# Optimization experiments

Hardware: AMD Instinct MI355X
Metric: run time of the kernel (lower is better)

The kernel has to match this reference:

```python
import jax, jax.numpy as jnp
import numpy as np

DIM = 1536; NH = 12; HD = 128; C2 = HD // 2          # rope half-dim = 64
F, H, W = 1, 30, 52
FRAME = H * W                                         # 1560 tokens/frame
SINK_FRAMES = 1; LOCAL_ATTN = 6
SINK = SINK_FRAMES * FRAME                            # 1560
MAX_ATTN = LOCAL_ATTN * 1560                          # 9360
CACHE = 9360                                          # kv cache length
GLOBAL_END = 9360; LOCAL_END_CACHE = 9360             # cache state before step
SPLITS = (C2 - 2 * (C2 // 3), C2 // 3, C2 // 3)       # (22, 21, 21)
EPS = 1e-6


def setup_inputs() -> dict:
    key = jax.random.key(0)
    ks = jax.random.split(key, 12)
    s = F * H * W
    rn = lambda k, sh, sc=1.0: jax.random.normal(k, sh, jnp.float32) * sc
    x = rn(ks[0], (1, s, DIM))
    Wq = rn(ks[1], (DIM, DIM), 0.02); Wk = rn(ks[2], (DIM, DIM), 0.02)
    Wv = rn(ks[3], (DIM, DIM), 0.02); Wo = rn(ks[4], (DIM, DIM), 0.02)
    zb = jnp.zeros((DIM,), jnp.float32)
    angles = jax.random.uniform(ks[5], (1024, C2), jnp.float32) * (2.0 * np.pi)
    freqs_cos = jnp.cos(angles); freqs_sin = jnp.sin(angles)
    cache_k = rn(ks[6], (1, CACHE, NH, HD)); cache_v = rn(ks[7], (1, CACHE, NH, HD))
    return dict(x=x, Wq=Wq, bq=zb, Wk=Wk, bk=zb, Wv=Wv, bv=zb, Wo=Wo, bo=zb,
                nq_w=jnp.ones((DIM,), jnp.float32), nk_w=jnp.ones((DIM,), jnp.float32),
                cache_k=cache_k, cache_v=cache_v,
                freqs_cos=freqs_cos, freqs_sin=freqs_sin,
                seq_lens=jnp.array([s], jnp.int32),
                grid_sizes=jnp.array([[F, H, W]], jnp.int32),
                current_start=GLOBAL_END)


def _rmsnorm(x, w):
    return x * jax.lax.rsqrt(jnp.mean(x * x, -1, keepdims=True) + EPS) * w


def _grid_table(table, start_frame):
    """table [1024, C2] -> per-token rope factors [S, 1, C2] over the (F,H,W) grid."""
    s0, s1, s2 = SPLITS
    tf, th, tw = table[:, :s0], table[:, s0:s0 + s1], table[:, s0 + s1:]
    fp = jnp.broadcast_to(tf[start_frame:start_frame + F][:, None, None, :], (F, H, W, s0))
    hp = jnp.broadcast_to(th[:H][None, :, None, :], (F, H, W, s1))
    wp = jnp.broadcast_to(tw[:W][None, None, :, :], (F, H, W, s2))
    return jnp.concatenate([fp, hp, wp], -1).reshape(F * H * W, 1, C2)


def _rope(x, cos, sin):
    # x: [b, s, n, d]; cos/sin: [s, 1, C2] (complex multiply in real arithmetic)
    b, s, n, d = x.shape
    xp = x.reshape(b, s, n, d // 2, 2)
    xr, xi = xp[..., 0], xp[..., 1]
    c, sn = cos[None], sin[None]                      # [1, s, 1, C2]
    out_r = xr * c - xi * sn
    out_i = xr * sn + xi * c
    return jnp.stack([out_r, out_i], -1).reshape(b, s, n, d)


def reference(x, Wq, bq, Wk, bk, Wv, bv, Wo, bo, nq_w, nk_w,
              cache_k, cache_v, freqs_cos, freqs_sin,
              seq_lens, grid_sizes, current_start):
    b, s = x.shape[:2]
    q = _rmsnorm(x @ Wq.T + bq, nq_w).reshape(b, s, NH, HD)
    k = _rmsnorm(x @ Wk.T + bk, nk_w).reshape(b, s, NH, HD)
    v = (x @ Wv.T + bv).reshape(b, s, NH, HD)

    start_frame = int(current_start) // FRAME
    cos = _grid_table(freqs_cos, start_frame)
    sin = _grid_table(freqs_sin, start_frame)
    rq = _rope(q, cos, sin)
    rk = _rope(k, cos, sin)

    # --- static cache bookkeeping (roll_and_insert path; all Python ints) ---
    num_new = s
    current_end = int(current_start) + num_new
    num_evicted = num_new + LOCAL_END_CACHE - CACHE           # 1560
    num_rolled = LOCAL_END_CACHE - num_evicted - SINK         # 6240
    local_end = LOCAL_END_CACHE + current_end - GLOBAL_END - num_evicted  # 9360
    local_start = local_end - num_new                         # 7800 == SINK + num_rolled
    temp_k = jnp.concatenate(
        [cache_k[:, :SINK], cache_k[:, SINK + num_evicted:SINK + num_evicted + num_rolled], rk], axis=1)
    temp_v = jnp.concatenate(
        [cache_v[:, :SINK], cache_v[:, SINK + num_evicted:SINK + num_evicted + num_rolled], v], axis=1)

    # --- sink + sliding-window attention ---
    local_budget = MAX_ATTN - SINK
    win_start = max(SINK, local_end - local_budget)
    k_cat = jnp.concatenate([temp_k[:, :SINK], temp_k[:, win_start:local_end]], axis=1)
    v_cat = jnp.concatenate([temp_v[:, :SINK], temp_v[:, win_start:local_end]], axis=1)

    logits = jnp.einsum('bqhd,bkhd->bhqk', rq, k_cat) * (HD ** -0.5)
    probs = jax.nn.softmax(logits, axis=-1)
    out = jnp.einsum('bhqk,bkhd->bqhd', probs, v_cat)
    y = out.reshape(b, s, DIM) @ Wo.T + bo
    return y
```

## Files before the change

### kernel.cpp

```cpp
#include <hip/hip_runtime.h>
#include <hip/hip_bf16.h>

typedef __bf16 bf16;
typedef __bf16 bf16x2 __attribute__((ext_vector_type(2)));
typedef __bf16 bf16x4 __attribute__((ext_vector_type(4)));
typedef __bf16 bf16x8 __attribute__((ext_vector_type(8)));
typedef float f32x4 __attribute__((ext_vector_type(4)));
typedef float f32x16 __attribute__((ext_vector_type(16)));
typedef unsigned u32x2 __attribute__((ext_vector_type(2)));

#define DIM 1536
#define NH 12
#define HD 128
#define SEQ 1560
#define KV 9360
#define KVP 9408
#define SINK 1560
#define NEWBASE 7800
#define QSCALE_L2E (0.08838834764831845f * 1.4426950408889634f)
#define NSPLIT 6
#define CHUNK 1568
#define NT 49
#define KB 32
#define QBLK 128
#define NQT 13

__device__ __forceinline__ void gl_lds16(const void* g, void* l) {
  __builtin_amdgcn_global_load_lds(
      (const __attribute__((address_space(1))) unsigned int*)g,
      (__attribute__((address_space(3))) unsigned int*)l, 16, 0, 0);
}

__device__ __forceinline__ f32x16 mfma32(bf16x8 a, bf16x8 b, f32x16 c) {
  return __builtin_amdgcn_mfma_f32_32x32x16_bf16(a, b, c, 0, 0, 0);
}

struct CastBatch {
  const float* src[5];
  bf16* dst[5];
  int n[5];
};
__global__ __launch_bounds__(256) void castall(CastBatch cb) {
  const float* src = cb.src[blockIdx.y];
  bf16* dst = cb.dst[blockIdx.y];
  int n = cb.n[blockIdx.y];
  int i = (blockIdx.x * 256 + threadIdx.x) * 8;
  if (i < n) {
    float4 a = *(const float4*)(src + i);
    float4 b = *(const float4*)(src + i + 4);
    bf16x8 o;
    o[0] = (bf16)a.x; o[1] = (bf16)a.y; o[2] = (bf16)a.z; o[3] = (bf16)a.w;
    o[4] = (bf16)b.x; o[5] = (bf16)b.y; o[6] = (bf16)b.z; o[7] = (bf16)b.w;
    *(bf16x8*)(dst + i) = o;
  }
}

__global__ __launch_bounds__(256) void clear_pad(bf16* __restrict__ Kcat,
                                                 bf16* __restrict__ Vt) {
  int h = blockIdx.y;
  int i = blockIdx.x * 256 + threadIdx.x;
  if (i < (KVP - KV) * HD) {
    int r = KV + i / HD, d = i % HD;
    Kcat[((size_t)h * KVP + r) * HD + d] = (bf16)0.f;
    int dv = i / (KVP - KV), j = KV + i % (KVP - KV);
    Vt[((size_t)h * HD + dv) * KVP + j] = (bf16)0.f;
  }
}

struct GemmBatch {
  const bf16* B[3];
  const float* bias[3];
  float* C[3];
};

#define BM 128
#define BN 128
#define BK 32

__global__ __launch_bounds__(256, 2) void gemm_bt(const bf16* __restrict__ A,
                                                  GemmBatch gb, int M) {
  const bf16* Bw = gb.B[blockIdx.z];
  const float* bias = gb.bias[blockIdx.z];
  float* C = gb.C[blockIdx.z];
  int bm = blockIdx.x * BM;
  int bn = blockIdx.y * BN;

  __shared__ bf16 Alds[2][BM][BK];
  __shared__ bf16 Blds[2][BN][BK];

  int t = threadIdx.x;
  int lane = t & 63;
  int wave = t >> 6;
  int wr = wave >> 1, wc = wave & 1;
  int fr = lane & 15;
  int fo = (lane >> 4) * 8;

  f32x4 acc[4][4] = {};

  const int NK = DIM / BK;
  int colA = (lane & 3) * 8;
  int lrow = lane >> 2;

#define STAGEG(buf, k0)                                                     \
  {                                                                         \
    _Pragma("unroll") for (int p = 0; p < 2; ++p) {                         \
      int rbase = wave * 16 + p * 64;                                       \
      int ga = bm + rbase + lrow;                                           \
      if (ga > M - 1) ga = M - 1;                                           \
      gl_lds16(A + (size_t)ga * DIM + (k0) + colA, &Alds[buf][rbase][0]);   \
      int gbv = bn + rbase + lrow;                                          \
      gl_lds16(Bw + (size_t)gbv * DIM + (k0) + colA, &Blds[buf][rbase][0]); \
    }                                                                       \
  }

  STAGEG(0, 0);
  int cur = 0;
  for (int ks = 0; ks < NK; ++ks) {
    __syncthreads();
    if (ks + 1 < NK) STAGEG(cur ^ 1, (ks + 1) * BK);
    bf16x8 af[4], bfv[4];
#pragma unroll
    for (int i = 0; i < 4; ++i)
      af[i] = *(const bf16x8*)&Alds[cur][wr * 64 + i * 16 + fr][fo];
#pragma unroll
    for (int j = 0; j < 4; ++j)
      bfv[j] = *(const bf16x8*)&Blds[cur][wc * 64 + j * 16 + fr][fo];
#pragma unroll
    for (int i = 0; i < 4; ++i)
#pragma unroll
      for (int j = 0; j < 4; ++j)
        acc[i][j] = __builtin_amdgcn_mfma_f32_16x16x32_bf16(af[i], bfv[j],
                                                            acc[i][j], 0, 0, 0);
    cur ^= 1;
  }
#undef STAGEG

  int g4 = (lane >> 4) * 4;
#pragma unroll
  for (int i = 0; i < 4; ++i) {
    int mbase = bm + wr * 64 + i * 16 + g4;
#pragma unroll
    for (int j = 0; j < 4; ++j) {
      int col = bn + wc * 64 + j * 16 + fr;
      float bv = bias[col];
#pragma unroll
      for (int r = 0; r < 4; ++r) {
        int m = mbase + r;
        if (m < M) C[(size_t)m * DIM + col] = acc[i][j][r] + bv;
      }
    }
  }
}

__global__ __launch_bounds__(256) void norm_rope(
    const float* __restrict__ qraw, const float* __restrict__ kraw,
    const float* __restrict__ nqw, const float* __restrict__ nkw,
    const float* __restrict__ fcos, const float* __restrict__ fsin,
    bf16* __restrict__ Qh, bf16* __restrict__ Kcat) {
  int tok = blockIdx.x;
  int tid = threadIdx.x;
  const float* qr = qraw + (size_t)tok * DIM;
  const float* kr = kraw + (size_t)tok * DIM;
  float sq = 0.f, sk = 0.f;
  for (int c = tid; c < DIM; c += 256) {
    float a = qr[c];
    sq += a * a;
    float b = kr[c];
    sk += b * b;
  }
#pragma unroll
  for (int off = 32; off; off >>= 1) {
    sq += __shfl_down(sq, off);
    sk += __shfl_down(sk, off);
  }
  __shared__ float red[2][4];
  int w = tid >> 6;
  if ((tid & 63) == 0) {
    red[0][w] = sq;
    red[1][w] = sk;
  }
  __syncthreads();
  sq = red[0][0] + red[0][1] + red[0][2] + red[0][3];
  sk = red[1][0] + red[1][1] + red[1][2] + red[1][3];
  float rsq = rsqrtf(sq * (1.0f / DIM) + 1e-6f);
  float rsk = rsqrtf(sk * (1.0f / DIM) + 1e-6f);

  int hrow = tok / 52, wrow = tok % 52;
  for (int p = tid; p < NH * 64; p += 256) {
    int n = p >> 6, i = p & 63;
    int trow = (i < 22) ? 6 : (i < 43 ? hrow : wrow);
    float cs = fcos[trow * 64 + i];
    float sn = fsin[trow * 64 + i];
    int c = n * HD + 2 * i;
    float xr = qr[c] * rsq * nqw[c];
    float xi = qr[c + 1] * rsq * nqw[c + 1];
    bf16x2 qo;
    qo[0] = (bf16)((xr * cs - xi * sn) * QSCALE_L2E);
    qo[1] = (bf16)((xr * sn + xi * cs) * QSCALE_L2E);
    *(bf16x2*)(Qh + ((size_t)n * SEQ + tok) * HD + 2 * i) = qo;
    float yr = kr[c] * rsk * nkw[c];
    float yi = kr[c + 1] * rsk * nkw[c + 1];
    bf16x2 ko;
    ko[0] = (bf16)(yr * cs - yi * sn);
    ko[1] = (bf16)(yr * sn + yi * cs);
    *(bf16x2*)(Kcat + ((size_t)n * KVP + NEWBASE + tok) * HD + 2 * i) = ko;
  }
}

__global__ __launch_bounds__(256) void build_kcat(const float* __restrict__ cache_k,
                                                  bf16* __restrict__ Kcat) {
  int j = blockIdx.x;
  int src = j < SINK ? j : j + SINK;
  const float* sp = cache_k + (size_t)src * DIM;
  for (int c4 = threadIdx.x; c4 < DIM / 4; c4 += 256) {
    float4 v = *(const float4*)(sp + c4 * 4);
    int c = c4 * 4;
    int n = c >> 7, d = c & 127;
    bf16x4 o;
    o[0] = (bf16)v.x; o[1] = (bf16)v.y; o[2] = (bf16)v.z; o[3] = (bf16)v.w;
    *(bf16x4*)(Kcat + ((size_t)n * KVP + j) * HD + d) = o;
  }
}

__global__ __launch_bounds__(256) void build_vt(const float* __restrict__ cache_v,
                                                const float* __restrict__ vraw,
                                                bf16* __restrict__ Vt) {
  int h = blockIdx.y;
  int j0 = blockIdx.x * 64;
  __shared__ bf16 T[128][72];
  int tid = threadIdx.x;
  for (int idx = tid; idx < 64 * 32; idx += 256) {
    int jl = idx >> 5, s = idx & 31;
    int j = j0 + jl;
    if (j >= KV) continue;
    const float* sp;
    if (j < NEWBASE) {
      int srcj = j < SINK ? j : j + SINK;
      sp = cache_v + (size_t)srcj * DIM + h * HD;
    } else {
      sp = vraw + (size_t)(j - NEWBASE) * DIM + h * HD;
    }
    float4 v = *(const float4*)(sp + s * 4);
    T[s * 4 + 0][jl] = (bf16)v.x;
    T[s * 4 + 1][jl] = (bf16)v.y;
    T[s * 4 + 2][jl] = (bf16)v.z;
    T[s * 4 + 3][jl] = (bf16)v.w;
  }
  __syncthreads();
  for (int idx = tid; idx < 128 * 16; idx += 256) {
    int d = idx >> 4, g = idx & 15;
    int j = j0 + g * 4;
    if (j + 4 > KV) continue;
    bf16x4 o;
    o[0] = T[d][4 * g];
    o[1] = T[d][4 * g + 1];
    o[2] = T[d][4 * g + 2];
    o[3] = T[d][4 * g + 3];
    *(bf16x4*)(Vt + ((size_t)h * HD + d) * KVP + j) = o;
  }
}

__global__ __launch_bounds__(256, 3) void attn_split(const bf16* __restrict__ Qh,
                                                     const bf16* __restrict__ Kcat,
                                                     const bf16* __restrict__ Vtg,
                                                     float* __restrict__ Opart,
                                                     float* __restrict__ MLpart) {
  int orig = blockIdx.x;
  int wgid = (orig & 7) * 117 + (orig >> 3);
  int qt = wgid % NQT;
  int rest = wgid / NQT;
  int h = rest % NH;
  int sp = rest / NH;
  int q0 = qt * QBLK;
  int c0 = sp * CHUNK;

  int t = threadIdx.x, lane = t & 63, w = t >> 6;
  int ql = lane & 31, hi = lane >> 5;

  __shared__ __align__(16) bf16 Klds[2][KB * 128];
  __shared__ __align__(16) bf16 Vlds[2][128 * KB];

  int qrow = q0 + w * 32 + ql;
  int qcl = qrow < SEQ ? qrow : SEQ - 1;
  const bf16* Qp = Qh + ((size_t)h * SEQ + qcl) * HD + hi * 8;
  bf16x8 qreg[8];
#pragma unroll
  for (int ks = 0; ks < 8; ++ks) qreg[ks] = *(const bf16x8*)(Qp + ks * 16);

  int kadd[2], vadd[2];
#pragma unroll
  for (int p = 0; p < 2; ++p) {
    int m = (2 * w + p) * 64 + lane;
    int rK = m >> 4, cK = m & 15;
    kadd[p] = rK * HD + (cK ^ (rK & 15)) * 8;
    int dV = m >> 2, cV = m & 3;
    vadd[p] = dV * KVP + (cV ^ ((dV >> 1) & 3)) * 8;
  }

  int koff[8];
#pragma unroll
  for (int ks = 0; ks < 8; ++ks)
    koff[ks] = ql * 256 + (((ks * 2 + hi) ^ (ql & 15)) * 16);
  int voff[4][2];
#pragma unroll
  for (int db = 0; db < 4; ++db)
#pragma unroll
    for (int ks = 0; ks < 2; ++ks)
      voff[db][ks] = (db * 32 + ql) * 64 + (((ks * 2 + hi) ^ ((ql >> 1) & 3)) * 16);

  const bf16* Khp = Kcat + (size_t)h * KVP * HD;
  const bf16* Vhp = Vtg + (size_t)h * HD * KVP;

  f32x16 oacc[4] = {};
  float m_q = -1e38f, l_q = 0.f;

#define STAGE(buf, j0)                                                        \
  {                                                                           \
    const bf16* Ks = Khp + (size_t)(j0)*HD;                                   \
    const bf16* Vs = Vhp + (j0);                                              \
    _Pragma("unroll") for (int p = 0; p < 2; ++p) {                           \
      gl_lds16(Ks + kadd[p], (char*)&Klds[buf][0] + w * 2048 + p * 1024);     \
      gl_lds16(Vs + vadd[p], (char*)&Vlds[buf][0] + w * 2048 + p * 1024);     \
    }                                                                         \
  }

  STAGE(0, c0);
  __syncthreads();
  int cur = 0;

  for (int ti = 0; ti < NT; ++ti) {
    int j0 = c0 + ti * KB;
    if (ti + 1 < NT) STAGE(cur ^ 1, j0 + KB);

    const char* Kc = (const char*)&Klds[cur][0];
    const char* Vc = (const char*)&Vlds[cur][0];

    f32x16 s0 = {};
    __builtin_amdgcn_s_setprio(1);
#pragma unroll
    for (int ks = 0; ks < 8; ++ks)
      s0 = mfma32(*(const bf16x8*)(Kc + koff[ks]), qreg[ks], s0);
    __builtin_amdgcn_s_setprio(0);

    if (j0 + KB > KV) {
#pragma unroll
      for (int reg = 0; reg < 16; ++reg) {
        int kk = (reg & 3) + 8 * (reg >> 2) + 4 * hi;
        if (j0 + kk >= KV) s0[reg] = -1e38f;
      }
    }

    float m8[8];
#pragma unroll
    for (int r = 0; r < 8; ++r) m8[r] = fmaxf(s0[r], s0[r + 8]);
    float mx = fmaxf(fmaxf(fmaxf(m8[0], m8[4]), fmaxf(m8[1], m8[5])),
                     fmaxf(fmaxf(m8[2], m8[6]), fmaxf(m8[3], m8[7])));
    mx = fmaxf(mx, __shfl_xor(mx, 32));

    if (__any(mx - m_q > 8.f)) {
      float mnew = fmaxf(m_q, mx);
      float corr = exp2f(m_q - mnew);
      m_q = mnew;
      l_q *= corr;
#pragma unroll
      for (int reg = 0; reg < 16; ++reg) {
        int qsrc = (reg & 3) + 8 * (reg >> 2) + 4 * hi;
        float c = __shfl(corr, qsrc);
#pragma unroll
        for (int db = 0; db < 4; ++db) oacc[db][reg] *= c;
      }
    }

#pragma unroll
    for (int r = 0; r < 16; ++r) s0[r] = exp2f(s0[r] - m_q);
    float t8[8];
#pragma unroll
    for (int r = 0; r < 8; ++r) t8[r] = s0[r] + s0[r + 8];
    float sum = ((t8[0] + t8[4]) + (t8[1] + t8[5])) +
                ((t8[2] + t8[6]) + (t8[3] + t8[7]));
    sum += __shfl_xor(sum, 32);
    l_q += sum;

    bf16x8 pa[2];
#pragma unroll
    for (int ks = 0; ks < 2; ++ks) {
      const int r0 = ks * 8;
      bf16x2 p0, p1, p2, p3;
      p0[0] = (bf16)s0[r0 + 0]; p0[1] = (bf16)s0[r0 + 1];
      p1[0] = (bf16)s0[r0 + 2]; p1[1] = (bf16)s0[r0 + 3];
      p2[0] = (bf16)s0[r0 + 4]; p2[1] = (bf16)s0[r0 + 5];
      p3[0] = (bf16)s0[r0 + 6]; p3[1] = (bf16)s0[r0 + 7];
      unsigned x0 = __builtin_bit_cast(unsigned, p0);
      unsigned x1 = __builtin_bit_cast(unsigned, p1);
      unsigned y0 = __builtin_bit_cast(unsigned, p2);
      unsigned y1 = __builtin_bit_cast(unsigned, p3);
      u32x2 r0v = __builtin_amdgcn_permlane32_swap(x0, y0, false, false);
      u32x2 r1v = __builtin_amdgcn_permlane32_swap(x1, y1, false, false);
      int4 tmp;
      tmp.x = (int)r0v[0];
      tmp.y = (int)r1v[0];
      tmp.z = (int)r0v[1];
      tmp.w = (int)r1v[1];
      pa[ks] = __builtin_bit_cast(bf16x8, tmp);
    }

    __builtin_amdgcn_s_setprio(1);
#pragma unroll
    for (int db = 0; db < 4; ++db)
#pragma unroll
      for (int ks = 0; ks < 2; ++ks)
        oacc[db] = mfma32(pa[ks], *(const bf16x8*)(Vc + voff[db][ks]), oacc[db]);
    __builtin_amdgcn_s_setprio(0);

    __syncthreads();
    cur ^= 1;
  }
#undef STAGE

  float* Oh = Opart + ((size_t)sp * NH + h) * SEQ * HD;
  float* MLh = MLpart + ((size_t)sp * NH + h) * SEQ * 2;
#pragma unroll
  for (int reg = 0; reg < 16; ++reg) {
    int q = q0 + w * 32 + (reg & 3) + 8 * (reg >> 2) + 4 * hi;
    if (q >= SEQ) continue;
#pragma unroll
    for (int db = 0; db < 4; ++db)
      Oh[(size_t)q * HD + db * 32 + ql] = oacc[db][reg];
  }
  if (lane < 32) {
    int q = q0 + w * 32 + ql;
    if (q < SEQ) {
      MLh[q * 2 + 0] = m_q;
      MLh[q * 2 + 1] = l_q;
    }
  }
}

__global__ __launch_bounds__(256) void attn_merge(const float* __restrict__ Opart,
                                                  const float* __restrict__ MLpart,
                                                  bf16* __restrict__ Aout) {
  int idx = blockIdx.x * 2 + (threadIdx.x >> 7);
  if (idx >= NH * SEQ) return;
  int d = threadIdx.x & 127;
  int h = idx / SEQ, q = idx % SEQ;
  float m[NSPLIT];
  float M = -1e38f;
#pragma unroll
  for (int s = 0; s < NSPLIT; ++s) {
    m[s] = MLpart[(((size_t)s * NH + h) * SEQ + q) * 2];
    M = fmaxf(M, m[s]);
  }
  float L = 0.f, o = 0.f;
#pragma unroll
  for (int s = 0; s < NSPLIT; ++s) {
    float wgt = exp2f(m[s] - M);
    L += MLpart[(((size_t)s * NH + h) * SEQ + q) * 2 + 1] * wgt;
    o += Opart[((((size_t)s * NH + h) * SEQ + q)) * HD + d] * wgt;
  }
  Aout[(size_t)q * DIM + h * HD + d] = (bf16)(o / L);
}

extern "C" void kernel_launch(void* const* d_in, const int* in_sizes, int n_in,
                              void* d_out, int out_size, void* d_ws, size_t ws_size,
                              hipStream_t stream) {
  const float* x = (const float*)d_in[0];
  const float* Wq = (const float*)d_in[1];
  const float* bq = (const float*)d_in[2];
  const float* Wk = (const float*)d_in[3];
  const float* bk = (const float*)d_in[4];
  const float* Wv = (const float*)d_in[5];
  const float* bv = (const float*)d_in[6];
  const float* Wo = (const float*)d_in[7];
  const float* bo = (const float*)d_in[8];
  const float* nqw = (const float*)d_in[9];
  const float* nkw = (const float*)d_in[10];
  const float* cache_k = (const float*)d_in[11];
  const float* cache_v = (const float*)d_in[12];
  const float* fcos = (const float*)d_in[13];
  const float* fsin = (const float*)d_in[14];
  float* out = (float*)d_out;

  char* ws = (char*)d_ws;
  size_t off = 0;
  auto alloc = [&](size_t bytes) {
    char* p = ws + off;
    off += (bytes + 255) & ~(size_t)255;
    return p;
  };
  const int XN = SEQ * DIM;
  const int WN = DIM * DIM;
  bf16* xb = (bf16*)alloc((size_t)XN * 2);
  bf16* Wqb = (bf16*)alloc((size_t)WN * 2);
  bf16* Wkb = (bf16*)alloc((size_t)WN * 2);
  bf16* Wvb = (bf16*)alloc((size_t)WN * 2);
  bf16* Wob = (bf16*)alloc((size_t)WN * 2);
  bf16* QhB = (bf16*)alloc((size_t)NH * SEQ * HD * 2);
  bf16* Kcat = (bf16*)alloc((size_t)NH * KVP * HD * 2);
  bf16* Vt = (bf16*)alloc((size_t)NH * HD * KVP * 2);
  bf16* Aout = (bf16*)alloc((size_t)XN * 2);
  float* MLpart = (float*)alloc((size_t)NSPLIT * NH * SEQ * 2 * 4);
  float* Opart = (float*)alloc((size_t)NSPLIT * NH * SEQ * HD * 4);
  float* qraw = Opart;
  float* kraw = qraw + XN;
  float* vraw = kraw + XN;

  CastBatch cb;
  cb.src[0] = x;  cb.dst[0] = xb;  cb.n[0] = XN;
  cb.src[1] = Wq; cb.dst[1] = Wqb; cb.n[1] = WN;
  cb.src[2] = Wk; cb.dst[2] = Wkb; cb.n[2] = WN;
  cb.src[3] = Wv; cb.dst[3] = Wvb; cb.n[3] = WN;
  cb.src[4] = Wo; cb.dst[4] = Wob; cb.n[4] = WN;
  castall<<<dim3((XN + 2047) / 2048, 5), 256, 0, stream>>>(cb);

  clear_pad<<<dim3(((KVP - KV) * HD + 255) / 256, NH), 256, 0, stream>>>(Kcat, Vt);

  GemmBatch gqkv;
  gqkv.B[0] = Wqb; gqkv.B[1] = Wkb; gqkv.B[2] = Wvb;
  gqkv.bias[0] = bq; gqkv.bias[1] = bk; gqkv.bias[2] = bv;
  gqkv.C[0] = qraw; gqkv.C[1] = kraw; gqkv.C[2] = vraw;
  gemm_bt<<<dim3(13, 12, 3), 256, 0, stream>>>(xb, gqkv, SEQ);

  norm_rope<<<SEQ, 256, 0, stream>>>(qraw, kraw, nqw, nkw, fcos, fsin, QhB, Kcat);
  build_kcat<<<NEWBASE, 256, 0, stream>>>(cache_k, Kcat);
  build_vt<<<dim3(147, NH), 256, 0, stream>>>(cache_v, vraw, Vt);

  attn_split<<<dim3(NQT * NH * NSPLIT), 256, 0, stream>>>(QhB, Kcat, Vt, Opart, MLpart);
  attn_merge<<<(NH * SEQ + 1) / 2, 256, 0, stream>>>(Opart, MLpart, Aout);

  GemmBatch gout;
  gout.B[0] = Wob; gout.B[1] = Wob; gout.B[2] = Wob;
  gout.bias[0] = bo; gout.bias[1] = bo; gout.bias[2] = bo;
  gout.C[0] = out; gout.C[1] = out; gout.C[2] = out;
  gemm_bt<<<dim3(13, 12, 1), 256, 0, stream>>>(Aout, gout, SEQ);
}
```

Measured before the change: 320.8 us.

## Load K tiles directly into registers and halve KV split count

The attention kernel stops staging K through LDS. Each lane loads its K fragment straight from global memory into registers, double-buffered across a 2x manually unrolled loop, while V still goes through LDS via async global-to-LDS loads. The KV split count drops from 6 to 3, doubling chunk length, occupancy drops from 3 to 2 waves-per-EU launch bound, and the XCD-aware block remap is adjusted for 468 workgroups. This cuts LDS traffic and the number of partial outputs to merge, at the cost of higher register pressure, fewer blocks for latency hiding, and uncoalesced per-lane K loads.

```diff
diff --git a/kernel.cpp b/kernel.cpp
--- a/kernel.cpp
+++ b/kernel.cpp
@@ -18,9 +18,9 @@
 #define SINK 1560
 #define NEWBASE 7800
 #define QSCALE_L2E (0.08838834764831845f * 1.4426950408889634f)
-#define NSPLIT 6
-#define CHUNK 1568
-#define NT 49
+#define NSPLIT 3
+#define CHUNK 3136
+#define NT 98
 #define KB 32
 #define QBLK 128
 #define NQT 13
@@ -260,24 +260,23 @@
   }
 }
 
-__global__ __launch_bounds__(256, 3) void attn_split(const bf16* __restrict__ Qh,
+__global__ __launch_bounds__(256, 2) void attn_split(const bf16* __restrict__ Qh,
                                                      const bf16* __restrict__ Kcat,
                                                      const bf16* __restrict__ Vtg,
                                                      float* __restrict__ Opart,
                                                      float* __restrict__ MLpart) {
   int orig = blockIdx.x;
-  int wgid = (orig & 7) * 117 + (orig >> 3);
+  int xcd = orig & 7, jj = orig >> 3;
+  int wgid = (xcd < 4 ? xcd * 59 : 236 + (xcd - 4) * 58) + jj;
   int qt = wgid % NQT;
-  int rest = wgid / NQT;
-  int h = rest % NH;
-  int sp = rest / NH;
+  int h = (wgid / NQT) % NH;
+  int sp = wgid / (NQT * NH);
   int q0 = qt * QBLK;
   int c0 = sp * CHUNK;
 
   int t = threadIdx.x, lane = t & 63, w = t >> 6;
   int ql = lane & 31, hi = lane >> 5;
 
-  __shared__ __align__(16) bf16 Klds[2][KB * 128];
   __shared__ __align__(16) bf16 Vlds[2][128 * KB];
 
   int qrow = q0 + w * 32 + ql;
@@ -287,20 +286,14 @@
 #pragma unroll
   for (int ks = 0; ks < 8; ++ks) qreg[ks] = *(const bf16x8*)(Qp + ks * 16);
 
-  int kadd[2], vadd[2];
+  int vadd[2];
 #pragma unroll
   for (int p = 0; p < 2; ++p) {
     int m = (2 * w + p) * 64 + lane;
-    int rK = m >> 4, cK = m & 15;
-    kadd[p] = rK * HD + (cK ^ (rK & 15)) * 8;
     int dV = m >> 2, cV = m & 3;
     vadd[p] = dV * KVP + (cV ^ ((dV >> 1) & 3)) * 8;
   }
 
-  int koff[8];
-#pragma unroll
-  for (int ks = 0; ks < 8; ++ks)
-    koff[ks] = ql * 256 + (((ks * 2 + hi) ^ (ql & 15)) * 16);
   int voff[4][2];
 #pragma unroll
   for (int db = 0; db < 4; ++db)
@@ -308,114 +301,118 @@
     for (int ks = 0; ks < 2; ++ks)
       voff[db][ks] = (db * 32 + ql) * 64 + (((ks * 2 + hi) ^ ((ql >> 1) & 3)) * 16);
 
-  const bf16* Khp = Kcat + (size_t)h * KVP * HD;
   const bf16* Vhp = Vtg + (size_t)h * HD * KVP;
+  const bf16* Kl0 = Kcat + (size_t)h * KVP * HD + (size_t)(c0 + ql) * HD + hi * 8;
 
   f32x16 oacc[4] = {};
   float m_q = -1e38f, l_q = 0.f;
 
-#define STAGE(buf, j0)                                                        \
+#define STAGEV(buf, j0v)                                                      \
   {                                                                           \
-    const bf16* Ks = Khp + (size_t)(j0)*HD;                                   \
-    const bf16* Vs = Vhp + (j0);                                              \
-    _Pragma("unroll") for (int p = 0; p < 2; ++p) {                           \
-      gl_lds16(Ks + kadd[p], (char*)&Klds[buf][0] + w * 2048 + p * 1024);     \
-      gl_lds16(Vs + vadd[p], (char*)&Vlds[buf][0] + w * 2048 + p * 1024);     \
+    const bf16* Vs = Vhp + (j0v);                                             \
+    _Pragma("unroll") for (int p = 0; p < 2; ++p)                             \
+        gl_lds16(Vs + vadd[p], (char*)&Vlds[buf][0] + w * 2048 + p * 1024);   \
+  }
+
+#define KLOAD(KR, TI)                                                         \
+  {                                                                           \
+    const bf16* Kl = Kl0 + (TI) * (KB * HD);                                  \
+    _Pragma("unroll") for (int ks = 0; ks < 8; ++ks)                          \
+        KR[ks] = *(const bf16x8*)(Kl + ks * 16);                              \
+  }
+
+#define TILE_BODY(KR, TI)                                                     \
+  {                                                                           \
+    int j0 = c0 + (TI)*KB;                                                    \
+    const char* Vc = (const char*)&Vlds[cur][0];                              \
+    f32x16 s0 = {};                                                           \
+    __builtin_amdgcn_s_setprio(1);                                            \
+    _Pragma("unroll") for (int ks = 0; ks < 8; ++ks)                          \
+        s0 = mfma32(KR[ks], qreg[ks], s0);                                    \
+    __builtin_amdgcn_s_setprio(0);                                            \
+    if (j0 + KB > KV) {                                                       \
+      _Pragma("unroll") for (int reg = 0; reg < 16; ++reg) {                  \
+        int kk = (reg & 3) + 8 * (reg >> 2) + 4 * hi;                         \
+        if (j0 + kk >= KV) s0[reg] = -1e38f;                                  \
+      }                                                                       \
     }                                                                         \
-  }
-
-  STAGE(0, c0);
+    float m8[8];                                                              \
+    _Pragma("unroll") for (int r = 0; r < 8; ++r)                             \
+        m8[r] = fmaxf(s0[r], s0[r + 8]);                                      \
+    float mx = fmaxf(fmaxf(fmaxf(m8[0], m8[4]), fmaxf(m8[1], m8[5])),         \
+                     fmaxf(fmaxf(m8[2], m8[6]), fmaxf(m8[3], m8[7])));        \
+    mx = fmaxf(mx, __shfl_xor(mx, 32));                                       \
+    if (__any(mx - m_q > 8.f)) {                                              \
+      float mnew = fmaxf(m_q, mx);                                            \
+      float corr = exp2f(m_q - mnew);                                         \
+      m_q = mnew;                                                             \
+      l_q *= corr;                                                            \
+      _Pragma("unroll") for (int reg = 0; reg < 16; ++reg) {                  \
+        int qsrc = (reg & 3) + 8 * (reg >> 2) + 4 * hi;                       \
+        float c = __shfl(corr, qsrc);                                         \
+        _Pragma("unroll") for (int db = 0; db < 4; ++db) oacc[db][reg] *= c;  \
+      }                                                                       \
+    }                                                                         \
+    _Pragma("unroll") for (int r = 0; r < 16; ++r)                            \
+        s0[r] = exp2f(s0[r] - m_q);                                           \
+    float t8[8];                                                              \
+    _Pragma("unroll") for (int r = 0; r < 8; ++r) t8[r] = s0[r] + s0[r + 8];  \
+    float sum = ((t8[0] + t8[4]) + (t8[1] + t8[5])) +                         \
+                ((t8[2] + t8[6]) + (t8[3] + t8[7]));                          \
+    sum += __shfl_xor(sum, 32);                                               \
+    l_q += sum;                                                               \
+    bf16x8 pa[2];                                                             \
+    _Pragma("unroll") for (int ks = 0; ks < 2; ++ks) {                        \
+      const int r0 = ks * 8;                                                  \
+      bf16x2 p0, p1, p2, p3;                                                  \
+      p0[0] = (bf16)s0[r0 + 0]; p0[1] = (bf16)s0[r0 + 1];                     \
+      p1[0] = (bf16)s0[r0 + 2]; p1[1] = (bf16)s0[r0 + 3];                     \
+      p2[0] = (bf16)s0[r0 + 4]; p2[1] = (bf16)s0[r0 + 5];                     \
+      p3[0] = (bf16)s0[r0 + 6]; p3[1] = (bf16)s0[r0 + 7];                     \
+      unsigned x0 = __builtin_bit_cast(unsigned, p0);                         \
+      unsigned x1 = __builtin_bit_cast(unsigned, p1);                         \
+      unsigned y0 = __builtin_bit_cast(unsigned, p2);                         \
+      unsigned y1 = __builtin_bit_cast(unsigned, p3);                         \
+      u32x2 r0v = __builtin_amdgcn_permlane32_swap(x0, y0, false, false);     \
+      u32x2 r1v = __builtin_amdgcn_permlane32_swap(x1, y1, false, false);     \
+      int4 tmp;                                                               \
+      tmp.x = (int)r0v[0];                                                    \
+      tmp.y = (int)r1v[0];                                                    \
+      tmp.z = (int)r0v[1];                                                    \
+      tmp.w = (int)r1v[1];                                                    \
+      pa[ks] = __builtin_bit_cast(bf16x8, tmp);                               \
+    }                                                                         \
+    __builtin_amdgcn_s_setprio(1);                                            \
+    _Pragma("unroll") for (int db = 0; db < 4; ++db)                          \
+        _Pragma("unroll") for (int ks = 0; ks < 2; ++ks)                      \
+            oacc[db] = mfma32(pa[ks], *(const bf16x8*)(Vc + voff[db][ks]),    \
+                              oacc[db]);                                      \
+    __builtin_amdgcn_s_setprio(0);                                            \
+    __syncthreads();                                                          \
+    cur ^= 1;                                                                 \
+  }
+
+  bf16x8 kA[8], kB[8];
+  STAGEV(0, c0);
+  KLOAD(kA, 0);
   __syncthreads();
   int cur = 0;
 
-  for (int ti = 0; ti < NT; ++ti) {
-    int j0 = c0 + ti * KB;
-    if (ti + 1 < NT) STAGE(cur ^ 1, j0 + KB);
-
-    const char* Kc = (const char*)&Klds[cur][0];
-    const char* Vc = (const char*)&Vlds[cur][0];
-
-    f32x16 s0 = {};
-    __builtin_amdgcn_s_setprio(1);
-#pragma unroll
-    for (int ks = 0; ks < 8; ++ks)
-      s0 = mfma32(*(const bf16x8*)(Kc + koff[ks]), qreg[ks], s0);
-    __builtin_amdgcn_s_setprio(0);
-
-    if (j0 + KB > KV) {
-#pragma unroll
-      for (int reg = 0; reg < 16; ++reg) {
-        int kk = (reg & 3) + 8 * (reg >> 2) + 4 * hi;
-        if (j0 + kk >= KV) s0[reg] = -1e38f;
-      }
+#pragma unroll 1
+  for (int it = 0; it < NT / 2; ++it) {
+    int ti = 2 * it;
+    STAGEV(cur ^ 1, c0 + (ti + 1) * KB);
+    KLOAD(kB, ti + 1);
+    TILE_BODY(kA, ti);
+    if (ti + 2 < NT) {
+      STAGEV(cur ^ 1, c0 + (ti + 2) * KB);
+      KLOAD(kA, ti + 2);
     }
-
-    float m8[8];
-#pragma unroll
-    for (int r = 0; r < 8; ++r) m8[r] = fmaxf(s0[r], s0[r + 8]);
-    float mx = fmaxf(fmaxf(fmaxf(m8[0], m8[4]), fmaxf(m8[1], m8[5])),
-                     fmaxf(fmaxf(m8[2], m8[6]), fmaxf(m8[3], m8[7])));
-    mx = fmaxf(mx, __shfl_xor(mx, 32));
-
-    if (__any(mx - m_q > 8.f)) {
-      float mnew = fmaxf(m_q, mx);
-      float corr = exp2f(m_q - mnew);
-      m_q = mnew;
-      l_q *= corr;
-#pragma unroll
-      for (int reg = 0; reg < 16; ++reg) {
-        int qsrc = (reg & 3) + 8 * (reg >> 2) + 4 * hi;
-        float c = __shfl(corr, qsrc);
-#pragma unroll
-        for (int db = 0; db < 4; ++db) oacc[db][reg] *= c;
-      }
-    }
-
-#pragma unroll
-    for (int r = 0; r < 16; ++r) s0[r] = exp2f(s0[r] - m_q);
-    float t8[8];
-#pragma unroll
-    for (int r = 0; r < 8; ++r) t8[r] = s0[r] + s0[r + 8];
-    float sum = ((t8[0] + t8[4]) + (t8[1] + t8[5])) +
-                ((t8[2] + t8[6]) + (t8[3] + t8[7]));
-    sum += __shfl_xor(sum, 32);
-    l_q += sum;
-
-    bf16x8 pa[2];
-#pragma unroll
-    for (int ks = 0; ks < 2; ++ks) {
-      const int r0 = ks * 8;
-      bf16x2 p0, p1, p2, p3;
-      p0[0] = (bf16)s0[r0 + 0]; p0[1] = (bf16)s0[r0 + 1];
-      p1[0] = (bf16)s0[r0 + 2]; p1[1] = (bf16)s0[r0 + 3];
-      p2[0] = (bf16)s0[r0 + 4]; p2[1] = (bf16)s0[r0 + 5];
-      p3[0] = (bf16)s0[r0 + 6]; p3[1] = (bf16)s0[r0 + 7];
-      unsigned x0 = __builtin_bit_cast(unsigned, p0);
-      unsigned x1 = __builtin_bit_cast(unsigned, p1);
-      unsigned y0 = __builtin_bit_cast(unsigned, p2);
-      unsigned y1 = __builtin_bit_cast(unsigned, p3);
-      u32x2 r0v = __builtin_amdgcn_permlane32_swap(x0, y0, false, false);
-      u32x2 r1v = __builtin_amdgcn_permlane32_swap(x1, y1, false, false);
-      int4 tmp;
-      tmp.x = (int)r0v[0];
-      tmp.y = (int)r1v[0];
-      tmp.z = (int)r0v[1];
-      tmp.w = (int)r1v[1];
-      pa[ks] = __builtin_bit_cast(bf16x8, tmp);
-    }
-
-    __builtin_amdgcn_s_setprio(1);
-#pragma unroll
-    for (int db = 0; db < 4; ++db)
-#pragma unroll
-      for (int ks = 0; ks < 2; ++ks)
-        oacc[db] = mfma32(pa[ks], *(const bf16x8*)(Vc + voff[db][ks]), oacc[db]);
-    __builtin_amdgcn_s_setprio(0);
-
-    __syncthreads();
-    cur ^= 1;
-  }
-#undef STAGE
+    TILE_BODY(kB, ti + 1);
+  }
+#undef TILE_BODY
+#undef KLOAD
+#undef STAGEV
 
   float* Oh = Opart + ((size_t)sp * NH + h) * SEQ * HD;
   float* MLh = MLpart + ((size_t)sp * NH + h) * SEQ * 2;
```

Result: slower. 352.2 us (+9.8%).

## Process two 32-row query tiles per wave to reuse K/V LDS fragments

Applied to the files above, without the earlier changes.

Each wave in the split attention kernel now handles 64 query rows as two independent 32-row tiles that share every K and V fragment read from LDS. This doubles the query block to 256 rows and cuts the number of workgroups, so K/V global-to-LDS traffic and LDS reads are amortised over twice the queries. In exchange, register pressure roughly doubles (two sets of accumulators and Q registers), occupancy drops to two workgroups per CU, and padding waste in the last query tile grows (1560 rows into 7 tiles of 256).

```diff
diff --git a/kernel.cpp b/kernel.cpp
--- a/kernel.cpp
+++ b/kernel.cpp
@@ -22,8 +22,8 @@
 #define CHUNK 1568
 #define NT 49
 #define KB 32
-#define QBLK 128
-#define NQT 13
+#define QBLK 256
+#define NQT 7
 
 __device__ __forceinline__ void gl_lds16(const void* g, void* l) {
   __builtin_amdgcn_global_load_lds(
@@ -260,13 +260,13 @@
   }
 }
 
-__global__ __launch_bounds__(256, 3) void attn_split(const bf16* __restrict__ Qh,
+__global__ __launch_bounds__(256, 2) void attn_split(const bf16* __restrict__ Qh,
                                                      const bf16* __restrict__ Kcat,
                                                      const bf16* __restrict__ Vtg,
                                                      float* __restrict__ Opart,
                                                      float* __restrict__ MLpart) {
   int orig = blockIdx.x;
-  int wgid = (orig & 7) * 117 + (orig >> 3);
+  int wgid = (orig & 7) * 63 + (orig >> 3);
   int qt = wgid % NQT;
   int rest = wgid / NQT;
   int h = rest % NH;
@@ -280,12 +280,19 @@
   __shared__ __align__(16) bf16 Klds[2][KB * 128];
   __shared__ __align__(16) bf16 Vlds[2][128 * KB];
 
-  int qrow = q0 + w * 32 + ql;
-  int qcl = qrow < SEQ ? qrow : SEQ - 1;
-  const bf16* Qp = Qh + ((size_t)h * SEQ + qcl) * HD + hi * 8;
-  bf16x8 qreg[8];
-#pragma unroll
-  for (int ks = 0; ks < 8; ++ks) qreg[ks] = *(const bf16x8*)(Qp + ks * 16);
+  bf16x8 qreg0[8], qreg1[8];
+  {
+    int qr0 = q0 + w * 64 + ql;
+    int qc0 = qr0 < SEQ ? qr0 : SEQ - 1;
+    const bf16* Qp0 = Qh + ((size_t)h * SEQ + qc0) * HD + hi * 8;
+#pragma unroll
+    for (int ks = 0; ks < 8; ++ks) qreg0[ks] = *(const bf16x8*)(Qp0 + ks * 16);
+    int qr1 = q0 + w * 64 + 32 + ql;
+    int qc1 = qr1 < SEQ ? qr1 : SEQ - 1;
+    const bf16* Qp1 = Qh + ((size_t)h * SEQ + qc1) * HD + hi * 8;
+#pragma unroll
+    for (int ks = 0; ks < 8; ++ks) qreg1[ks] = *(const bf16x8*)(Qp1 + ks * 16);
+  }
 
   int kadd[2], vadd[2];
 #pragma unroll
@@ -311,8 +318,9 @@
   const bf16* Khp = Kcat + (size_t)h * KVP * HD;
   const bf16* Vhp = Vtg + (size_t)h * HD * KVP;
 
-  f32x16 oacc[4] = {};
-  float m_q = -1e38f, l_q = 0.f;
+  f32x16 oacc0[4] = {}, oacc1[4] = {};
+  float m_q0 = -1e38f, l_q0 = 0.f;
+  float m_q1 = -1e38f, l_q1 = 0.f;
 
 #define STAGE(buf, j0)                                                        \
   {                                                                           \
@@ -324,10 +332,33 @@
     }                                                                         \
   }
 
+#define PACK(SRC, PA)                                                         \
+  _Pragma("unroll") for (int ks = 0; ks < 2; ++ks) {                          \
+    const int r0 = ks * 8;                                                    \
+    bf16x2 p0, p1, p2, p3;                                                    \
+    p0[0] = (bf16)SRC[r0 + 0]; p0[1] = (bf16)SRC[r0 + 1];                     \
+    p1[0] = (bf16)SRC[r0 + 2]; p1[1] = (bf16)SRC[r0 + 3];                     \
+    p2[0] = (bf16)SRC[r0 + 4]; p2[1] = (bf16)SRC[r0 + 5];                     \
+    p3[0] = (bf16)SRC[r0 + 6]; p3[1] = (bf16)SRC[r0 + 7];                     \
+    unsigned x0 = __builtin_bit_cast(unsigned, p0);                           \
+    unsigned x1 = __builtin_bit_cast(unsigned, p1);                           \
+    unsigned y0 = __builtin_bit_cast(unsigned, p2);                           \
+    unsigned y1 = __builtin_bit_cast(unsigned, p3);                           \
+    u32x2 r0v = __builtin_amdgcn_permlane32_swap(x0, y0, false, false);       \
+    u32x2 r1v = __builtin_amdgcn_permlane32_swap(x1, y1, false, false);       \
+    int4 tmp;                                                                 \
+    tmp.x = (int)r0v[0];                                                      \
+    tmp.y = (int)r1v[0];                                                      \
+    tmp.z = (int)r0v[1];                                                      \
+    tmp.w = (int)r1v[1];                                                      \
+    PA[ks] = __builtin_bit_cast(bf16x8, tmp);                                 \
+  }
+
   STAGE(0, c0);
   __syncthreads();
   int cur = 0;
 
+#pragma unroll 1
   for (int ti = 0; ti < NT; ++ti) {
     int j0 = c0 + ti * KB;
     if (ti + 1 < NT) STAGE(cur ^ 1, j0 + KB);
@@ -335,103 +366,130 @@
     const char* Kc = (const char*)&Klds[cur][0];
     const char* Vc = (const char*)&Vlds[cur][0];
 
-    f32x16 s0 = {};
+    f32x16 s0 = {}, s1 = {};
     __builtin_amdgcn_s_setprio(1);
 #pragma unroll
-    for (int ks = 0; ks < 8; ++ks)
-      s0 = mfma32(*(const bf16x8*)(Kc + koff[ks]), qreg[ks], s0);
+    for (int ks = 0; ks < 8; ++ks) {
+      bf16x8 kf = *(const bf16x8*)(Kc + koff[ks]);
+      s0 = mfma32(kf, qreg0[ks], s0);
+      s1 = mfma32(kf, qreg1[ks], s1);
+    }
     __builtin_amdgcn_s_setprio(0);
 
     if (j0 + KB > KV) {
 #pragma unroll
       for (int reg = 0; reg < 16; ++reg) {
         int kk = (reg & 3) + 8 * (reg >> 2) + 4 * hi;
-        if (j0 + kk >= KV) s0[reg] = -1e38f;
+        if (j0 + kk >= KV) {
+          s0[reg] = -1e38f;
+          s1[reg] = -1e38f;
+        }
       }
     }
 
-    float m8[8];
-#pragma unroll
-    for (int r = 0; r < 8; ++r) m8[r] = fmaxf(s0[r], s0[r + 8]);
-    float mx = fmaxf(fmaxf(fmaxf(m8[0], m8[4]), fmaxf(m8[1], m8[5])),
-                     fmaxf(fmaxf(m8[2], m8[6]), fmaxf(m8[3], m8[7])));
-    mx = fmaxf(mx, __shfl_xor(mx, 32));
-
-    if (__any(mx - m_q > 8.f)) {
-      float mnew = fmaxf(m_q, mx);
-      float corr = exp2f(m_q - mnew);
-      m_q = mnew;
-      l_q *= corr;
+    float mx0, mx1;
+    {
+      float m8[8];
+#pragma unroll
+      for (int r = 0; r < 8; ++r) m8[r] = fmaxf(s0[r], s0[r + 8]);
+      float mx = fmaxf(fmaxf(fmaxf(m8[0], m8[4]), fmaxf(m8[1], m8[5])),
+                       fmaxf(fmaxf(m8[2], m8[6]), fmaxf(m8[3], m8[7])));
+      mx0 = fmaxf(mx, __shfl_xor(mx, 32));
+#pragma unroll
+      for (int r = 0; r < 8; ++r) m8[r] = fmaxf(s1[r], s1[r + 8]);
+      mx = fmaxf(fmaxf(fmaxf(m8[0], m8[4]), fmaxf(m8[1], m8[5])),
+                 fmaxf(fmaxf(m8[2], m8[6]), fmaxf(m8[3], m8[7])));
+      mx1 = fmaxf(mx, __shfl_xor(mx, 32));
+    }
+
+    if (__any(fmaxf(mx0 - m_q0, mx1 - m_q1) > 8.f)) {
+      float mn0 = fmaxf(m_q0, mx0);
+      float c0r = exp2f(m_q0 - mn0);
+      m_q0 = mn0;
+      l_q0 *= c0r;
+      float mn1 = fmaxf(m_q1, mx1);
+      float c1r = exp2f(m_q1 - mn1);
+      m_q1 = mn1;
+      l_q1 *= c1r;
 #pragma unroll
       for (int reg = 0; reg < 16; ++reg) {
         int qsrc = (reg & 3) + 8 * (reg >> 2) + 4 * hi;
-        float c = __shfl(corr, qsrc);
-#pragma unroll
-        for (int db = 0; db < 4; ++db) oacc[db][reg] *= c;
+        float ca = __shfl(c0r, qsrc);
+        float cb = __shfl(c1r, qsrc);
+#pragma unroll
+        for (int db = 0; db < 4; ++db) {
+          oacc0[db][reg] *= ca;
+          oacc1[db][reg] *= cb;
+        }
       }
     }
 
-#pragma unroll
-    for (int r = 0; r < 16; ++r) s0[r] = exp2f(s0[r] - m_q);
-    float t8[8];
-#pragma unroll
-    for (int r = 0; r < 8; ++r) t8[r] = s0[r] + s0[r + 8];
-    float sum = ((t8[0] + t8[4]) + (t8[1] + t8[5])) +
-                ((t8[2] + t8[6]) + (t8[3] + t8[7]));
-    sum += __shfl_xor(sum, 32);
-    l_q += sum;
-
-    bf16x8 pa[2];
-#pragma unroll
-    for (int ks = 0; ks < 2; ++ks) {
-      const int r0 = ks * 8;
-      bf16x2 p0, p1, p2, p3;
-      p0[0] = (bf16)s0[r0 + 0]; p0[1] = (bf16)s0[r0 + 1];
-      p1[0] = (bf16)s0[r0 + 2]; p1[1] = (bf16)s0[r0 + 3];
-      p2[0] = (bf16)s0[r0 + 4]; p2[1] = (bf16)s0[r0 + 5];
-      p3[0] = (bf16)s0[r0 + 6]; p3[1] = (bf16)s0[r0 + 7];
-      unsigned x0 = __builtin_bit_cast(unsigned, p0);
-      unsigned x1 = __builtin_bit_cast(unsigned, p1);
-      unsigned y0 = __builtin_bit_cast(unsigned, p2);
-      unsigned y1 = __builtin_bit_cast(unsigned, p3);
-      u32x2 r0v = __builtin_amdgcn_permlane32_swap(x0, y0, false, false);
-      u32x2 r1v = __builtin_amdgcn_permlane32_swap(x1, y1, false, false);
-      int4 tmp;
-      tmp.x = (int)r0v[0];
-      tmp.y = (int)r1v[0];
-      tmp.z = (int)r0v[1];
-      tmp.w = (int)r1v[1];
-      pa[ks] = __builtin_bit_cast(bf16x8, tmp);
+    bf16x8 pa0[2], pa1[2];
+    {
+#pragma unroll
+      for (int r = 0; r < 16; ++r) s0[r] = exp2f(s0[r] - m_q0);
+      float t8[8];
+#pragma unroll
+      for (int r = 0; r < 8; ++r) t8[r] = s0[r] + s0[r + 8];
+      float sum = ((t8[0] + t8[4]) + (t8[1] + t8[5])) +
+                  ((t8[2] + t8[6]) + (t8[3] + t8[7]));
+      sum += __shfl_xor(sum, 32);
+      l_q0 += sum;
+      PACK(s0, pa0);
+#pragma unroll
+      for (int r = 0; r < 16; ++r) s1[r] = exp2f(s1[r] - m_q1);
+#pragma unroll
+      for (int r = 0; r < 8; ++r) t8[r] = s1[r] + s1[r + 8];
+      sum = ((t8[0] + t8[4]) + (t8[1] + t8[5])) +
+            ((t8[2] + t8[6]) + (t8[3] + t8[7]));
+      sum += __shfl_xor(sum, 32);
+      l_q1 += sum;
+      PACK(s1, pa1);
     }
 
     __builtin_amdgcn_s_setprio(1);
 #pragma unroll
     for (int db = 0; db < 4; ++db)
 #pragma unroll
-      for (int ks = 0; ks < 2; ++ks)
-        oacc[db] = mfma32(pa[ks], *(const bf16x8*)(Vc + voff[db][ks]), oacc[db]);
+      for (int ks = 0; ks < 2; ++ks) {
+        bf16x8 vf = *(const bf16x8*)(Vc + voff[db][ks]);
+        oacc0[db] = mfma32(pa0[ks], vf, oacc0[db]);
+        oacc1[db] = mfma32(pa1[ks], vf, oacc1[db]);
+      }
     __builtin_amdgcn_s_setprio(0);
 
     __syncthreads();
     cur ^= 1;
   }
+#undef PACK
 #undef STAGE
 
   float* Oh = Opart + ((size_t)sp * NH + h) * SEQ * HD;
   float* MLh = MLpart + ((size_t)sp * NH + h) * SEQ * 2;
 #pragma unroll
   for (int reg = 0; reg < 16; ++reg) {
-    int q = q0 + w * 32 + (reg & 3) + 8 * (reg >> 2) + 4 * hi;
-    if (q >= SEQ) continue;
-#pragma unroll
-    for (int db = 0; db < 4; ++db)
-      Oh[(size_t)q * HD + db * 32 + ql] = oacc[db][reg];
+    int qb = q0 + w * 64 + (reg & 3) + 8 * (reg >> 2) + 4 * hi;
+    if (qb < SEQ) {
+#pragma unroll
+      for (int db = 0; db < 4; ++db)
+        Oh[(size_t)qb * HD + db * 32 + ql] = oacc0[db][reg];
+    }
+    int qb1 = qb + 32;
+    if (qb1 < SEQ) {
+#pragma unroll
+      for (int db = 0; db < 4; ++db)
+        Oh[(size_t)qb1 * HD + db * 32 + ql] = oacc1[db][reg];
+    }
   }
   if (lane < 32) {
-    int q = q0 + w * 32 + ql;
+    int q = q0 + w * 64 + ql;
     if (q < SEQ) {
-      MLh[q * 2 + 0] = m_q;
-      MLh[q * 2 + 1] = l_q;
+      MLh[q * 2 + 0] = m_q0;
+      MLh[q * 2 + 1] = l_q0;
+    }
+    if (q + 32 < SEQ) {
+      MLh[(q + 32) * 2 + 0] = m_q1;
+      MLh[(q + 32) * 2 + 1] = l_q1;
     }
   }
 }
```

Result: slower. 342.8 us (+6.9%).
